# Optimization experiments

Measured on AMD Instinct MI355X. Metric: run time of the kernel, lower is better.

## Reference

```python
import jax, jax.numpy as jnp
import numpy as np

B, L, H, NE, P, E, R = 4, 1024, 256, 64, 512, 65536, 4
V, DW, DC, DT, DD, REL = 200000, 100, 20, 20, 20, 97
N = B * NE          # flat entity-node count
D2 = 2 * H          # rnn_output_size (BiLSTM concat)
DBI = H + DD        # bilinear input dim (hidden + dis_size)
DIN = DW + DC + DT  # word + coref + ner embedding concat


def setup_inputs():
    key = jax.random.key(0)
    ks = jax.random.split(key, 32)
    g = lambda i, shape, s: jax.random.normal(ks[i], shape, dtype=jnp.float32) * s
    return {
        "e_mapping": jax.random.uniform(ks[0], (B, NE, L), dtype=jnp.float32) / L,
        "word_table": g(1, (V, DW), 0.1),
        "coref_table": g(2, (L, DC), 0.1),
        "ner_table": g(3, (13, DT), 0.1),
        "Wi_f": g(4, (DIN, 4 * H), 0.05), "Wh_f": g(5, (H, 4 * H), 0.05), "b_f": jnp.zeros((4 * H,), jnp.float32),
        "Wi_b": g(6, (DIN, 4 * H), 0.05), "Wh_b": g(7, (H, 4 * H), 0.05), "b_b": jnp.zeros((4 * H,), jnp.float32),
        "W_rel": g(8, (R, D2, D2), 0.02),
        "W_self_h": g(9, (D2, D2), 0.02), "W_msg_h": g(10, (D2, D2), 0.02), "b_h": jnp.zeros((D2,), jnp.float32),
        "W_self_t": g(11, (D2, D2), 0.02), "W_msg_t": g(12, (D2, D2), 0.02), "b_t": jnp.zeros((D2,), jnp.float32),
        "head_W": g(13, (D2, H), 0.02), "head_b": jnp.zeros((H,), jnp.float32),
        "tail_W": g(14, (D2, H), 0.02), "tail_b": jnp.zeros((H,), jnp.float32),
        "dis_table": g(15, (20, DD), 0.1),
        "bili_W": g(16, (DBI, DBI, H), 0.02), "bili_b": jnp.zeros((H,), jnp.float32),
        "out_W": g(17, (2 * H, REL), 0.02), "out_b": jnp.zeros((REL,), jnp.float32),
        "context_idxs": jax.random.randint(ks[18], (B, L), 0, V),
        "pos": jax.random.randint(ks[19], (B, L), 0, L),
        "context_ner": jax.random.randint(ks[20], (B, L), 0, 13),
        "hts": jax.random.randint(ks[21], (B, P, 2), 0, NE),
        "dis_h_2_t": jax.random.randint(ks[22], (B, P), 0, 20),
        "dis_t_2_h": jax.random.randint(ks[23], (B, P), 0, 20),
        "edge_src": jax.random.randint(ks[24], (E,), 0, N),
        "edge_dst": jax.random.randint(ks[25], (E,), 0, N),
        "edge_type": jax.random.randint(ks[26], (E,), 0, R),
    }


def _lstm_dir(x, Wi, Wh, b):
    # x: [L, B, D] -> hidden sequence [L, B, H]
    Bz = x.shape[1]
    def step(carry, xt):
        h, c = carry
        gates = xt @ Wi + h @ Wh + b
        i, f, gg, o = jnp.split(gates, 4, axis=-1)
        c = jax.nn.sigmoid(f) * c + jax.nn.sigmoid(i) * jnp.tanh(gg)
        h = jax.nn.sigmoid(o) * jnp.tanh(c)
        return (h, c), h
    init = (jnp.zeros((Bz, H), x.dtype), jnp.zeros((Bz, H), x.dtype))
    _, hs = jax.lax.scan(step, init, x)
    return hs


def reference(e_mapping, word_table, coref_table, ner_table,
              Wi_f, Wh_f, b_f, Wi_b, Wh_b, b_b,
              W_rel, W_self_h, W_msg_h, b_h, W_self_t, W_msg_t, b_t,
              head_W, head_b, tail_W, tail_b, dis_table,
              bili_W, bili_b, out_W, out_b,
              context_idxs, pos, context_ner, hts, dis_h_2_t, dis_t_2_h,
              edge_src, edge_dst, edge_type):
    # STEP 1: embed + BiLSTM document encoder
    sent_emb = jnp.concatenate([word_table[context_idxs], coref_table[pos],
                                ner_table[context_ner]], axis=-1)   # [B,L,DIN]
    x = jnp.transpose(sent_emb, (1, 0, 2))                          # [L,B,DIN]
    hf = _lstm_dir(x, Wi_f, Wh_f, b_f)
    hb = _lstm_dir(x[::-1], Wi_b, Wh_b, b_b)[::-1]
    docs_rep = jnp.transpose(jnp.concatenate([hf, hb], -1), (1, 0, 2))  # [B,L,2H]
    # KEGRL layer: entity pooling (e_mapping @ docs_rep) + relation-typed GNN
    ent = jnp.einsum('bel,bld->bed', e_mapping, docs_rep).reshape(N, D2)
    m = jax.nn.relu(jnp.einsum('nd,rde->rne', ent, W_rel))          # per-rel node msgs [R,N,D2]
    msgs = m[edge_type, edge_src]                                   # irregular gather [E,D2]
    agg = jax.ops.segment_sum(msgs, edge_dst, num_segments=N)       # scatter-add [N,D2]
    hs = jax.nn.relu(ent @ W_self_h + agg @ W_msg_h + b_h).reshape(B, NE, D2)
    ts = jax.nn.relu(ent @ W_self_t + agg @ W_msg_t + b_t).reshape(B, NE, D2)
    # get_ht: gather head/tail entity reps for each candidate pair
    bidx = jnp.arange(B)[:, None]
    h = hs[bidx, hts[..., 0]]                                       # [B,P,D2]
    t = ts[bidx, hts[..., 1]]
    hp = h @ head_W + head_b                                        # [B,P,H]
    tp = t @ tail_W + tail_b
    # bilinear scoring with distance embeddings
    hd = jnp.concatenate([hp, dis_table[dis_h_2_t]], -1)            # [B,P,H+DD]
    td = jnp.concatenate([tp, dis_table[dis_t_2_h]], -1)
    bl = jax.nn.relu(jnp.einsum('bpi,ijk,bpj->bpk', hd, bili_W, td) + bili_b)
    logits = jnp.concatenate([bl, hp * tp], -1) @ out_W + out_b     # [B,P,REL]
    return logits
```

## Files before the change

kernel.cpp:

```cpp
#include <hip/hip_runtime.h>
#include <cstdint>

#define B_   4
#define L_   1024
#define H_   256
#define NE_  64
#define P_   512
#define E_   65536
#define R_   4
#define DW_  100
#define DC_  20
#define DT_  20
#define DD_  20
#define REL_ 97
#define N_   256
#define D2_  512
#define DBI_ 276
#define DIN_ 140
#define G4_  1024

#define OFF_EMB  0u
#define OFF_PRE  573440u
#define OFF_DOCS 8962048u
#define OFF_WHP  11059200u
#define OFF_ENT  11321344u
#define OFF_M    11452416u
#define OFF_AGG  11976704u
#define OFF_HS   12107776u
#define OFF_TS   12238848u
#define OFF_HD   12369920u
#define OFF_TD   12935168u
#define OFF_HPTP 13500416u
#define OFF_BL   14024704u
#define OFF_WB_F16   0u
#define OFF_HDB_F16  10174464u
#define OFF_TDB_F16  10469376u

typedef _Float16 h2v __attribute__((ext_vector_type(2)));
typedef _Float16 h8v __attribute__((ext_vector_type(8)));
typedef float f4v __attribute__((ext_vector_type(4)));
typedef unsigned int u4v __attribute__((ext_vector_type(4)));

union AFrag { h8v v; h2v h[4]; };
union TDreg { u4v u; h2v h[4]; };

__device__ __forceinline__ unsigned short f16bits(float x) {
    return __builtin_bit_cast(unsigned short, (_Float16)x);
}

#if __has_builtin(__builtin_amdgcn_exp2f)
#define EXP2F __builtin_amdgcn_exp2f
#else
#define EXP2F exp2f
#endif
#if __has_builtin(__builtin_amdgcn_rcpf)
#define RCPF __builtin_amdgcn_rcpf
#else
#define RCPF(x) (1.0f / (x))
#endif

__device__ __forceinline__ float fast_sig(float x) {
    return RCPF(1.0f + EXP2F(x * -1.44269504f));
}
__device__ __forceinline__ float fast_tanh(float x) {
    return 1.0f - 2.0f * RCPF(EXP2F(x * 2.88539008f) + 1.0f);
}

__device__ __forceinline__ f4v MF(h8v a, u4v b, f4v c) {
    return __builtin_amdgcn_mfma_f32_16x16x32_f16(
        a, __builtin_bit_cast(h8v, b), c, 0, 0, 0);
}

__global__ __launch_bounds__(192) void k_embed(
    const float* __restrict__ wt, const float* __restrict__ ct,
    const float* __restrict__ nt, const int* __restrict__ widx,
    const int* __restrict__ pidx, const int* __restrict__ nidx,
    float* __restrict__ emb) {
    int row = blockIdx.x;
    int t = threadIdx.x;
    if (t >= DIN_) return;
    float v;
    if (t < DW_)            v = wt[(size_t)widx[row] * DW_ + t];
    else if (t < DW_ + DC_) v = ct[pidx[row] * DC_ + (t - DW_)];
    else                    v = nt[nidx[row] * DT_ + (t - DW_ - DC_)];
    emb[(size_t)row * DIN_ + t] = v;
}

__global__ __launch_bounds__(256) void k_pack_wh(
    const float* __restrict__ whf, const float* __restrict__ whb,
    unsigned* __restrict__ whp) {
    unsigned gid = blockIdx.x * 256 + threadIdx.x;
    unsigned m    = gid & 3u;
    unsigned lane = (gid >> 2) & 63u;
    unsigned kk   = (gid >> 8) & 7u;
    unsigned n    = (gid >> 11) & 63u;
    unsigned dir  = gid >> 17;
    const float* src = dir ? whb : whf;
    unsigned k0  = kk * 32u + (lane >> 4) * 8u + 2u * m;
    unsigned col = n * 16u + (lane & 15u);
    unsigned lo = f16bits(src[(size_t)k0 * G4_ + col]);
    unsigned hi = f16bits(src[(size_t)(k0 + 1) * G4_ + col]);
    whp[gid] = (hi << 16) | lo;
}

__global__ __launch_bounds__(256) void k_pregates(
    const float* __restrict__ emb,
    const float* __restrict__ wif, const float* __restrict__ bf,
    const float* __restrict__ wib, const float* __restrict__ bb,
    float* __restrict__ pre) {
    int dir = blockIdx.y;
    const float* Wi   = dir ? wib : wif;
    const float* bias = dir ? bb : bf;
    int x8 = blockIdx.x * 8;
    __shared__ float se[8 * DIN_];
    for (int idx = threadIdx.x; idx < 8 * DIN_; idx += 256)
        se[idx] = emb[(size_t)(x8 + idx / DIN_) * DIN_ + idx % DIN_];
    __syncthreads();
    int t = threadIdx.x;
    float acc[8][4];
#pragma unroll
    for (int r = 0; r < 8; r++)
#pragma unroll
        for (int q = 0; q < 4; q++) acc[r][q] = bias[t + q * 256];
    for (int k = 0; k < DIN_; k++) {
        float w0 = Wi[k * G4_ + t];
        float w1 = Wi[k * G4_ + t + 256];
        float w2 = Wi[k * G4_ + t + 512];
        float w3 = Wi[k * G4_ + t + 768];
#pragma unroll
        for (int r = 0; r < 8; r++) {
            float e = se[r * DIN_ + k];
            acc[r][0] += e * w0; acc[r][1] += e * w1;
            acc[r][2] += e * w2; acc[r][3] += e * w3;
        }
    }
#pragma unroll
    for (int r = 0; r < 8; r++) {
        float* dst = pre + ((size_t)(dir * 4096 + x8 + r)) * G4_ + t;
        dst[0] = acc[r][0]; dst[256] = acc[r][1];
        dst[512] = acc[r][2]; dst[768] = acc[r][3];
    }
}

__global__ __launch_bounds__(512)
__attribute__((amdgpu_waves_per_eu(2)))
void k_lstm(
    const float* __restrict__ pre, const unsigned* __restrict__ whb,
    float* __restrict__ docs) {
    int dir = blockIdx.x >> 2, b = blockIdx.x & 3;
    int tid = threadIdx.x;
    int w = tid >> 6;
    int lane = tid & 63, q = lane >> 4, c = lane & 15;
    __shared__ alignas(16) u4v wl[16][8][64];
    __shared__ alignas(16) unsigned hbuf[2][128];
    const float* pb = pre + (size_t)(dir * 4 + b) * (1024 * 1024);
    const u4v* wsrc = (const u4v*)whb + (size_t)dir * 32768;

    u4v wr[2][3][8];
#pragma unroll
    for (int j2 = 0; j2 < 2; j2++)
#pragma unroll
        for (int gt = 0; gt < 3; gt++)
#pragma unroll
            for (int kk = 0; kk < 8; kk++)
                wr[j2][gt][kk] =
                    wsrc[(size_t)((2 * w + j2 + 16 * gt) * 8 + kk) * 64 + lane];
#pragma unroll
    for (int j2 = 0; j2 < 2; j2++)
#pragma unroll
        for (int kk = 0; kk < 8; kk++)
            wl[2 * w + j2][kk][lane] =
                wsrc[(size_t)((2 * w + j2 + 48) * 8 + kk) * 64 + lane];
    if (tid < 256) ((unsigned*)hbuf)[tid] = 0;

    bool is_act = (q < 2);
    int j2a = q & 1;
    int u_act = 32 * w + 16 * j2a + c;
    float cst = 0.f;
    __syncthreads();

#pragma unroll 1
    for (int t = 0; t < L_; ++t) {
        int row = dir ? (L_ - 1 - t) : t;
        int cur = t & 1;
        float pr0, pr1, pr2, pr3;
        if (is_act) {
            const float* prow = pb + (size_t)row * 1024 + u_act;
            pr0 = prow[0]; pr1 = prow[256]; pr2 = prow[512]; pr3 = prow[768];
        }
        const u4v* hb4 = (const u4v*)&hbuf[cur][0];
        f4v a00 = (f4v)0.f, a01 = (f4v)0.f, a02 = (f4v)0.f, a03 = (f4v)0.f;
        f4v a10 = (f4v)0.f, a11 = (f4v)0.f, a12 = (f4v)0.f, a13 = (f4v)0.f;
#pragma unroll
        for (int kk = 0; kk < 8; kk++) {
            h8v a = __builtin_bit_cast(h8v, hb4[kk * 4 + q]);
            u4v l0 = wl[2 * w][kk][lane];
            u4v l1 = wl[2 * w + 1][kk][lane];
            a00 = MF(a, wr[0][0][kk], a00);
            a01 = MF(a, wr[0][1][kk], a01);
            a02 = MF(a, wr[0][2][kk], a02);
            a03 = MF(a, l0, a03);
            a10 = MF(a, wr[1][0][kk], a10);
            a11 = MF(a, wr[1][1][kk], a11);
            a12 = MF(a, wr[1][2][kk], a12);
            a13 = MF(a, l1, a13);
        }
        if (is_act) {
            float ig = (j2a ? a10.x : a00.x) + pr0;
            float fg = (j2a ? a11.x : a01.x) + pr1;
            float gg = (j2a ? a12.x : a02.x) + pr2;
            float og = (j2a ? a13.x : a03.x) + pr3;
            float si = fast_sig(ig), sf = fast_sig(fg), so = fast_sig(og);
            cst = sf * cst + si * fast_tanh(gg);
            float h = so * fast_tanh(cst);
            ((_Float16*)hbuf)[(cur ^ 1) * 256 + u_act] = (_Float16)h;
            docs[((size_t)(b * L_ + row)) * D2_ + dir * H_ + u_act] = h;
        }
        __syncthreads();
    }
}

__global__ __launch_bounds__(256) void k_pool(
    const float* __restrict__ emap, const float* __restrict__ docs,
    float* __restrict__ ent) {
    int n = blockIdx.x;
    int b = n >> 6;
    __shared__ float sm[1024];
    for (int idx = threadIdx.x; idx < 1024; idx += 256)
        sm[idx] = emap[(size_t)n * 1024 + idx];
    __syncthreads();
    int d = threadIdx.x;
    float a0 = 0.f, a1 = 0.f;
    const float* db = docs + (size_t)b * L_ * D2_;
#pragma unroll 4
    for (int l = 0; l < L_; l++) {
        float mv = sm[l];
        a0 += mv * db[l * D2_ + d];
        a1 += mv * db[l * D2_ + d + 256];
    }
    ent[n * D2_ + d] = a0;
    ent[n * D2_ + d + 256] = a1;
}

__global__ __launch_bounds__(256) void k_cvt_w(
    const float* __restrict__ W, unsigned short* __restrict__ Wb) {
    unsigned gid = blockIdx.x * 256 + threadIdx.x;
    unsigned t = gid & 7u;
    unsigned np = (gid >> 3) & 15u;
    unsigned q = (gid >> 7) & 3u;
    unsigned ns = (gid >> 9) & 15u;
    unsigned c = gid >> 13;
    unsigned i = c / 9u, jc = c - i * 9u;
    unsigned jp = jc * 32u + q * 8u + t;
    float v = (jp < 276u) ? W[((size_t)i * 276u + jp) * 256u + ns * 16u + np] : 0.f;
    Wb[gid] = f16bits(v);
}

__global__ __launch_bounds__(256) void k_msg(
    const float* __restrict__ ent, const float* __restrict__ wrel,
    float* __restrict__ m) {
    int n = blockIdx.x, r = blockIdx.y;
    __shared__ float se[512];
    for (int idx = threadIdx.x; idx < 512; idx += 256) se[idx] = ent[n * D2_ + idx];
    __syncthreads();
    int d = threadIdx.x;
    const float* W = wrel + (size_t)r * D2_ * D2_;
    float a0 = 0.f, a1 = 0.f;
#pragma unroll 4
    for (int k = 0; k < 512; k++) {
        float e = se[k];
        a0 += e * W[k * 512 + d];
        a1 += e * W[k * 512 + d + 256];
    }
    size_t o = ((size_t)(r * N_ + n)) * D2_;
    m[o + d] = fmaxf(a0, 0.f);
    m[o + d + 256] = fmaxf(a1, 0.f);
}

__global__ __launch_bounds__(256) void k_scatter(
    const int* __restrict__ esrc, const int* __restrict__ edst,
    const int* __restrict__ etyp, const float* __restrict__ m,
    float* __restrict__ agg) {
    int gid = blockIdx.x * 256 + threadIdx.x;
    int e = gid >> 7, q = (gid & 127) << 2;
    int s = esrc[e], dn = edst[e], ty = etyp[e];
    const float4 v = *(const float4*)(m + ((size_t)(ty * N_ + s)) * D2_ + q);
    float* ap = agg + (size_t)dn * D2_ + q;
    atomicAdd(ap + 0, v.x); atomicAdd(ap + 1, v.y);
    atomicAdd(ap + 2, v.z); atomicAdd(ap + 3, v.w);
}

__global__ __launch_bounds__(256) void k_hsts(
    const float* __restrict__ ent, const float* __restrict__ agg,
    const float* __restrict__ wsh, const float* __restrict__ wmh, const float* __restrict__ bh,
    const float* __restrict__ wst, const float* __restrict__ wmt, const float* __restrict__ bt,
    float* __restrict__ hs, float* __restrict__ ts) {
    int n = blockIdx.x, ty = blockIdx.y;
    const float* Ws = ty ? wst : wsh;
    const float* Wm = ty ? wmt : wmh;
    const float* bi = ty ? bt : bh;
    float* out = ty ? ts : hs;
    __shared__ float se[512], sa[512];
    for (int idx = threadIdx.x; idx < 512; idx += 256) {
        se[idx] = ent[n * 512 + idx];
        sa[idx] = agg[n * 512 + idx];
    }
    __syncthreads();
    int d = threadIdx.x;
    float a0 = bi[d], a1 = bi[d + 256];
#pragma unroll 2
    for (int k = 0; k < 512; k++) {
        float e = se[k], a = sa[k];
        a0 += e * Ws[k * 512 + d] + a * Wm[k * 512 + d];
        a1 += e * Ws[k * 512 + d + 256] + a * Wm[k * 512 + d + 256];
    }
    out[n * 512 + d] = fmaxf(a0, 0.f);
    out[n * 512 + d + 256] = fmaxf(a1, 0.f);
}

__global__ __launch_bounds__(256) void k_pairs(
    const float* __restrict__ hs, const float* __restrict__ ts,
    const int* __restrict__ hts, const int* __restrict__ dht, const int* __restrict__ dth,
    const float* __restrict__ hW, const float* __restrict__ hb,
    const float* __restrict__ tW, const float* __restrict__ tb,
    const float* __restrict__ dis,
    unsigned short* __restrict__ hdb, unsigned short* __restrict__ tdb,
    float* __restrict__ hptp) {
    int bp = blockIdx.x;
    int b = bp >> 9;
    int hi = hts[bp * 2], ti = hts[bp * 2 + 1];
    __shared__ float sh[512], st[512];
    const float* hr = hs + ((size_t)(b * NE_ + hi)) * D2_;
    const float* tr = ts + ((size_t)(b * NE_ + ti)) * D2_;
    for (int idx = threadIdx.x; idx < 512; idx += 256) {
        sh[idx] = hr[idx];
        st[idx] = tr[idx];
    }
    __syncthreads();
    int d = threadIdx.x;
    float ah = hb[d], at = tb[d];
#pragma unroll 4
    for (int k = 0; k < 512; k++) {
        ah += sh[k] * hW[k * H_ + d];
        at += st[k] * tW[k * H_ + d];
    }
    size_t rb = (size_t)bp * 288;
    hdb[rb + d] = f16bits(ah);
    tdb[rb + d] = f16bits(at);
    hptp[(size_t)bp * H_ + d] = ah * at;
    if (d < DD_) {
        hdb[rb + 256 + d] = f16bits(dis[dht[bp] * DD_ + d]);
        tdb[rb + 256 + d] = f16bits(dis[dth[bp] * DD_ + d]);
    }
    if (d < 12) {
        hdb[rb + 276 + d] = 0;
        tdb[rb + 276 + d] = 0;
    }
}

__global__ __launch_bounds__(512) void k_bili(
    const unsigned short* __restrict__ Wb, const unsigned short* __restrict__ hdb,
    const unsigned short* __restrict__ tdb, float* __restrict__ blacc) {
    int bx = blockIdx.x, kc = blockIdx.y;
    int i0 = kc * 17 + (kc < 4 ? kc : 4);
    int cnt = 17 + (kc < 4 ? 1 : 0);
    int steps = cnt * 9;
    int tid = threadIdx.x;
    int w = tid >> 6, lane = tid & 63, q = lane >> 4, n16 = lane & 15;

    __shared__ alignas(16) unsigned short Bs[2][8192];
    __shared__ unsigned short hds[128 * 18];

    for (int e = tid; e < 128 * 18; e += 512)
        hds[e] = hdb[(size_t)(bx * 128 + e / 18) * 288 + i0 + e % 18];

    int p = bx * 128 + w * 16 + n16;
    const u4v* tdsrc = (const u4v*)(tdb + (size_t)p * 288);
    TDreg td[9];
#pragma unroll
    for (int jc = 0; jc < 9; jc++) td[jc].u = tdsrc[jc * 4 + q];

    f4v acc[16];
#pragma unroll
    for (int i = 0; i < 16; i++) acc[i] = (f4v)0.f;

    const u4v* gsrc = (const u4v*)Wb + (size_t)(i0 * 9) * 1024 + tid * 2;
    u4v r0 = gsrc[0], r1 = gsrc[1];
    {
        u4v* bs0 = (u4v*)(&Bs[0][0]);
        bs0[tid * 2] = r0; bs0[tid * 2 + 1] = r1;
    }
    __syncthreads();

    int il = 0, jc = 0;
    for (int s = 0; s < steps; s++) {
        if (s + 1 < steps) {
            const u4v* gs = gsrc + (size_t)(s + 1) * 1024;
            r0 = gs[0]; r1 = gs[1];
        }
        unsigned short hraw = hds[(w * 16 + n16) * 18 + il];
        _Float16 hv = __builtin_bit_cast(_Float16, hraw);
        h2v hd2 = {hv, hv};
        AFrag af;
#pragma unroll
        for (int e2 = 0; e2 < 4; e2++) af.h[e2] = hd2 * td[jc].h[e2];
        const unsigned short* bsc = &Bs[s & 1][0];
#pragma unroll
        for (int ns = 0; ns < 16; ns++) {
            h8v bf = *(const h8v*)(bsc + ns * 512 + lane * 8);
            acc[ns] = __builtin_amdgcn_mfma_f32_16x16x32_f16(af.v, bf, acc[ns], 0, 0, 0);
        }
        if (s + 1 < steps) {
            u4v* bsn = (u4v*)(&Bs[(s + 1) & 1][0]);
            bsn[tid * 2] = r0; bsn[tid * 2 + 1] = r1;
        }
        __syncthreads();
        if (++jc == 9) { jc = 0; il++; }
    }

    float* dst = blacc + (size_t)(bx * 128 + w * 16 + q * 4) * 256 + n16;
#pragma unroll
    for (int ns = 0; ns < 16; ns++)
#pragma unroll
        for (int r = 0; r < 4; r++)
            atomicAdd(dst + (size_t)r * 256 + ns * 16, acc[ns][r]);
}

__global__ __launch_bounds__(128) void k_final(
    const float* __restrict__ blacc, const float* __restrict__ bib,
    const float* __restrict__ hptp,
    const float* __restrict__ oW, const float* __restrict__ ob,
    float* __restrict__ out) {
    int bp = blockIdx.x;
    __shared__ float s[512];
    for (int idx = threadIdx.x; idx < 512; idx += 128)
        s[idx] = (idx < 256) ? fmaxf(blacc[(size_t)bp * 256 + idx] + bib[idx], 0.f)
                             : hptp[(size_t)bp * 256 + idx - 256];
    __syncthreads();
    int r = threadIdx.x;
    if (r >= REL_) return;
    float a = ob[r];
#pragma unroll 4
    for (int d = 0; d < 512; d++) a += s[d] * oW[d * REL_ + r];
    out[(size_t)bp * REL_ + r] = a;
}

extern "C" void kernel_launch(void* const* d_in, const int* in_sizes, int n_in,
                              void* d_out, int out_size, void* d_ws, size_t ws_size,
                              hipStream_t stream) {
    const float* e_map    = (const float*)d_in[0];
    const float* word_t   = (const float*)d_in[1];
    const float* coref_t  = (const float*)d_in[2];
    const float* ner_t    = (const float*)d_in[3];
    const float* Wi_f     = (const float*)d_in[4];
    const float* Wh_f     = (const float*)d_in[5];
    const float* b_f      = (const float*)d_in[6];
    const float* Wi_b     = (const float*)d_in[7];
    const float* Wh_b     = (const float*)d_in[8];
    const float* b_b      = (const float*)d_in[9];
    const float* W_rel    = (const float*)d_in[10];
    const float* W_self_h = (const float*)d_in[11];
    const float* W_msg_h  = (const float*)d_in[12];
    const float* b_h      = (const float*)d_in[13];
    const float* W_self_t = (const float*)d_in[14];
    const float* W_msg_t  = (const float*)d_in[15];
    const float* b_t      = (const float*)d_in[16];
    const float* head_W   = (const float*)d_in[17];
    const float* head_b   = (const float*)d_in[18];
    const float* tail_W   = (const float*)d_in[19];
    const float* tail_b   = (const float*)d_in[20];
    const float* dis_t    = (const float*)d_in[21];
    const float* bili_W   = (const float*)d_in[22];
    const float* bili_b   = (const float*)d_in[23];
    const float* out_W    = (const float*)d_in[24];
    const float* out_b    = (const float*)d_in[25];
    const int* ctx_idx = (const int*)d_in[26];
    const int* pos     = (const int*)d_in[27];
    const int* ctx_ner = (const int*)d_in[28];
    const int* hts     = (const int*)d_in[29];
    const int* dht     = (const int*)d_in[30];
    const int* dth     = (const int*)d_in[31];
    const int* esrc    = (const int*)d_in[32];
    const int* edst    = (const int*)d_in[33];
    const int* etyp    = (const int*)d_in[34];

    float* ws = (float*)d_ws;
    float* emb  = ws + OFF_EMB;
    float* pre  = ws + OFF_PRE;
    float* docs = ws + OFF_DOCS;
    unsigned* whp = (unsigned*)(ws + OFF_WHP);
    float* ent  = ws + OFF_ENT;
    float* m    = ws + OFF_M;
    float* agg  = ws + OFF_AGG;
    float* hsb  = ws + OFF_HS;
    float* tsb  = ws + OFF_TS;
    float* hptp = ws + OFF_HPTP;
    float* blacc = ws + OFF_BL;
    unsigned short* Wb  = (unsigned short*)(ws + OFF_WB_F16);
    unsigned short* hdb = (unsigned short*)(ws + OFF_HDB_F16);
    unsigned short* tdb = (unsigned short*)(ws + OFF_TDB_F16);
    float* out  = (float*)d_out;

    hipLaunchKernelGGL(k_embed, dim3(B_ * L_), dim3(192), 0, stream,
                       word_t, coref_t, ner_t, ctx_idx, pos, ctx_ner, emb);
    hipLaunchKernelGGL(k_pack_wh, dim3(1024), dim3(256), 0, stream, Wh_f, Wh_b, whp);
    hipLaunchKernelGGL(k_pregates, dim3(512, 2), dim3(256), 0, stream,
                       emb, Wi_f, b_f, Wi_b, b_b, pre);
    hipLaunchKernelGGL(k_lstm, dim3(8), dim3(512), 0, stream, pre, whp, docs);
    hipLaunchKernelGGL(k_pool, dim3(N_), dim3(256), 0, stream, e_map, docs, ent);
    hipLaunchKernelGGL(k_cvt_w, dim3(79488), dim3(256), 0, stream, bili_W, Wb);
    hipLaunchKernelGGL(k_msg, dim3(N_, R_), dim3(256), 0, stream, ent, W_rel, m);
    hipMemsetAsync(agg, 0, (size_t)N_ * D2_ * sizeof(float), stream);
    hipLaunchKernelGGL(k_scatter, dim3(E_ * 128 / 256), dim3(256), 0, stream,
                       esrc, edst, etyp, m, agg);
    hipLaunchKernelGGL(k_hsts, dim3(N_, 2), dim3(256), 0, stream,
                       ent, agg, W_self_h, W_msg_h, b_h, W_self_t, W_msg_t, b_t, hsb, tsb);
    hipLaunchKernelGGL(k_pairs, dim3(B_ * P_), dim3(256), 0, stream,
                       hsb, tsb, hts, dht, dth, head_W, head_b, tail_W, tail_b,
                       dis_t, hdb, tdb, hptp);
    hipMemsetAsync(blacc, 0, (size_t)2048 * 256 * sizeof(float), stream);
    hipLaunchKernelGGL(k_bili, dim3(16, 16), dim3(512), 0, stream, Wb, hdb, tdb, blacc);
    hipLaunchKernelGGL(k_final, dim3(B_ * P_), dim3(128), 0, stream,
                       blacc, bili_b, hptp, out_W, out_b, out);
}
```

Before: 2.589 ms.

## Replace atomic scatter-add with CSR build and per-node gather reduction

Builds a destination-sorted edge list on device with a counting pass, a prefix scan and a fill kernel. Each node then sums its incoming message rows in a single block without atomics. This targets the contention cost of tens of millions of float atomicAdds onto only 256 destination rows. In exchange it adds three small launches and reuses part of the workspace for index buffers, and the summation order now varies between runs.

```diff
diff --git a/kernel.cpp b/kernel.cpp
--- a/kernel.cpp
+++ b/kernel.cpp
@@ -277,17 +277,56 @@
     m[o + d + 256] = fmaxf(a1, 0.f);
 }
 
-__global__ __launch_bounds__(256) void k_scatter(
-    const int* __restrict__ esrc, const int* __restrict__ edst,
-    const int* __restrict__ etyp, const float* __restrict__ m,
+__global__ __launch_bounds__(256) void k_sc_count(
+    const int* __restrict__ edst, int* __restrict__ cnt, int* __restrict__ pos) {
+    int e = blockIdx.x * 256 + threadIdx.x;
+    pos[e] = atomicAdd(&cnt[edst[e]], 1);
+}
+
+__global__ __launch_bounds__(256) void k_sc_scan(
+    const int* __restrict__ cnt, int* __restrict__ offs) {
+    __shared__ int s[256];
+    int t = threadIdx.x;
+    int my = cnt[t];
+    s[t] = my;
+    __syncthreads();
+    for (int d = 1; d < 256; d <<= 1) {
+        int v = (t >= d) ? s[t - d] : 0;
+        __syncthreads();
+        s[t] += v;
+        __syncthreads();
+    }
+    offs[t] = s[t] - my;
+}
+
+__global__ __launch_bounds__(256) void k_sc_fill(
+    const int* __restrict__ edst, const int* __restrict__ offs,
+    const int* __restrict__ pos, int* __restrict__ slot) {
+    int e = blockIdx.x * 256 + threadIdx.x;
+    slot[offs[edst[e]] + pos[e]] = e;
+}
+
+__global__ __launch_bounds__(512) void k_sc_agg(
+    const int* __restrict__ esrc, const int* __restrict__ etyp,
+    const int* __restrict__ cnt, const int* __restrict__ offs,
+    const int* __restrict__ slot, const float* __restrict__ m,
     float* __restrict__ agg) {
-    int gid = blockIdx.x * 256 + threadIdx.x;
-    int e = gid >> 7, q = (gid & 127) << 2;
-    int s = esrc[e], dn = edst[e], ty = etyp[e];
-    const float4 v = *(const float4*)(m + ((size_t)(ty * N_ + s)) * D2_ + q);
-    float* ap = agg + (size_t)dn * D2_ + q;
-    atomicAdd(ap + 0, v.x); atomicAdd(ap + 1, v.y);
-    atomicAdd(ap + 2, v.z); atomicAdd(ap + 3, v.w);
+    int n = blockIdx.x, tid = threadIdx.x;
+    __shared__ int sbase[128];
+    int c0 = offs[n], c = cnt[n];
+    float acc = 0.f;
+    for (int i0 = 0; i0 < c; i0 += 128) {
+        int chunk = min(128, c - i0);
+        if (tid < chunk) {
+            int e = slot[c0 + i0 + tid];
+            sbase[tid] = (etyp[e] * N_ + esrc[e]) * D2_;
+        }
+        __syncthreads();
+        for (int j = 0; j < chunk; j++)
+            acc += m[(size_t)sbase[j] + tid];
+        __syncthreads();
+    }
+    agg[(size_t)n * D2_ + tid] = acc;
 }
 
 __global__ __launch_bounds__(256) void k_hsts(
@@ -499,6 +538,11 @@
     unsigned short* Wb  = (unsigned short*)(ws + OFF_WB_F16);
     unsigned short* hdb = (unsigned short*)(ws + OFF_HDB_F16);
     unsigned short* tdb = (unsigned short*)(ws + OFF_TDB_F16);
+    int* aux   = (int*)(ws + OFF_HD);
+    int* cnt_  = aux;
+    int* posb  = aux + 256;
+    int* slot  = aux + 256 + E_;
+    int* offs  = aux + 256 + 2 * E_;
     float* out  = (float*)d_out;
 
     hipLaunchKernelGGL(k_embed, dim3(B_ * L_), dim3(192), 0, stream,
@@ -510,9 +554,14 @@
     hipLaunchKernelGGL(k_pool, dim3(N_), dim3(256), 0, stream, e_map, docs, ent);
     hipLaunchKernelGGL(k_cvt_w, dim3(79488), dim3(256), 0, stream, bili_W, Wb);
     hipLaunchKernelGGL(k_msg, dim3(N_, R_), dim3(256), 0, stream, ent, W_rel, m);
-    hipMemsetAsync(agg, 0, (size_t)N_ * D2_ * sizeof(float), stream);
-    hipLaunchKernelGGL(k_scatter, dim3(E_ * 128 / 256), dim3(256), 0, stream,
-                       esrc, edst, etyp, m, agg);
+    hipMemsetAsync(cnt_, 0, 256 * sizeof(int), stream);
+    hipLaunchKernelGGL(k_sc_count, dim3(E_ / 256), dim3(256), 0, stream,
+                       edst, cnt_, posb);
+    hipLaunchKernelGGL(k_sc_scan, dim3(1), dim3(256), 0, stream, cnt_, offs);
+    hipLaunchKernelGGL(k_sc_fill, dim3(E_ / 256), dim3(256), 0, stream,
+                       edst, offs, posb, slot);
+    hipLaunchKernelGGL(k_sc_agg, dim3(N_), dim3(512), 0, stream,
+                       esrc, etyp, cnt_, offs, slot, m, agg);
     hipLaunchKernelGGL(k_hsts, dim3(N_, 2), dim3(256), 0, stream,
                        ent, agg, W_self_h, W_msg_h, b_h, W_self_t, W_msg_t, b_t, hsb, tsb);
     hipLaunchKernelGGL(k_pairs, dim3(B_ * P_), dim3(256), 0, stream,
```

After: 2.208 ms. 14.7% less time.
